# Performance work log

Hardware: AMD Instinct MI355X
Metric: run time of the kernel (lower is better)

The kernel has to match this reference:

```python
import jax, jax.numpy as jnp
import numpy as np

DIM = 384
NUM_HEADS = 12
WS = 7
POSMLP_DIM = 32
HEAD_DIM = DIM // NUM_HEADS
SCALE = HEAD_DIM ** -0.5


def setup_inputs() -> dict:
    key = jax.random.key(0)
    ks = jax.random.split(key, 10)
    B_ = 2048
    N = WS * WS
    nW = 64
    inp = {
        "x": jax.random.normal(ks[0], (B_, N, DIM), dtype=jnp.float32),
        "mask": jax.random.normal(ks[1], (nW, N, N), dtype=jnp.float32),
        # qkv Linear: weight [3*dim, dim], bias [3*dim]
        "qkv_w": jax.random.normal(ks[2], (3 * DIM, DIM), dtype=jnp.float32) * (DIM ** -0.5),
        "qkv_b": jax.random.normal(ks[3], (3 * DIM,), dtype=jnp.float32) * 0.02,
        # proj Linear
        "proj_w": jax.random.normal(ks[4], (DIM, DIM), dtype=jnp.float32) * (DIM ** -0.5),
        "proj_b": jax.random.normal(ks[5], (DIM,), dtype=jnp.float32) * 0.02,
        # posmlp: Conv2d(2, posmlp_dim, 1) -> ReLU -> Conv2d(posmlp_dim, num_heads, 1)
        "pm_w1": jax.random.normal(ks[6], (POSMLP_DIM, 2), dtype=jnp.float32) * 0.5,
        "pm_b1": jax.random.normal(ks[7], (POSMLP_DIM,), dtype=jnp.float32) * 0.02,
        "pm_w2": jax.random.normal(ks[8], (NUM_HEADS, POSMLP_DIM), dtype=jnp.float32) * (POSMLP_DIM ** -0.5),
        "pm_b2": jax.random.normal(ks[9], (NUM_HEADS,), dtype=jnp.float32) * 0.02,
    }
    return inp


def _pos_bias(pm_w1, pm_b1, pm_w2, pm_b2):
    # pos_hw: [2, N] with channel 0 = row index, channel 1 = col index
    coords = jnp.arange(WS, dtype=jnp.float32)
    pos_h = jnp.repeat(coords[:, None], WS, axis=1).reshape(-1)  # row idx
    pos_w = jnp.tile(coords[None, :], (WS, 1)).reshape(-1)       # col idx
    pos = jnp.stack([pos_h, pos_w], axis=0)                      # [2, N]
    # pos_input[c, i, j] = pos[c, j] - pos[c, i]  (unsqueeze(2) - unsqueeze(3))
    d = pos[:, None, :] - pos[:, :, None]                        # [2, N, N]
    d = jnp.sign(d) * jnp.log1p(jnp.abs(d))
    # 1x1 convs == per-position channel MLP
    h = jax.nn.relu(jnp.einsum("cij,oc->oij", d, pm_w1) + pm_b1[:, None, None])
    bias = jnp.einsum("cij,oc->oij", h, pm_w2) + pm_b2[:, None, None]  # [H, N, N]
    return bias


def reference(x, mask, qkv_w, qkv_b, proj_w, proj_b, pm_w1, pm_b1, pm_w2, pm_b2):
    B_, N, C = x.shape
    H = NUM_HEADS
    qkv = x @ qkv_w.T + qkv_b                                     # [B_, N, 3C]
    qkv = qkv.reshape(B_, N, 3, H, C // H).transpose(2, 0, 3, 1, 4)
    q, k, v = qkv[0], qkv[1], qkv[2]                              # [B_, H, N, d]
    attn = jnp.einsum("bhnd,bhmd->bhnm", q * SCALE, k)            # [B_, H, N, N]
    attn = attn + _pos_bias(pm_w1, pm_b1, pm_w2, pm_b2)[None]
    nW = mask.shape[0]
    attn = attn.reshape(B_ // nW, nW, H, N, N) + mask[None, :, None]
    attn = jax.nn.softmax(attn.reshape(B_, H, N, N), axis=-1)
    out = jnp.einsum("bhnm,bhmd->bhnd", attn, v)                  # [B_, H, N, d]
    out = out.transpose(0, 2, 1, 3).reshape(B_, N, C)
    return out @ proj_w.T + proj_b
```

## Files before the change

### kernel.cpp

```cpp
#include <hip/hip_runtime.h>
#include <hip/hip_bf16.h>
#include <stdint.h>

#define DIM 384
#define QKVN 1152
#define NHEAD 12
#define HDIM 32
#define NTOK 49
#define NWIN 2048
static constexpr float SCALE_Q = 0.17677669529663687f;

typedef float f32x4 __attribute__((ext_vector_type(4)));
typedef float f32x4u __attribute__((ext_vector_type(4), aligned(4)));
typedef __bf16 bf16x8 __attribute__((ext_vector_type(8)));
typedef unsigned short u16;
typedef u16 u16x8 __attribute__((ext_vector_type(8)));
typedef u16 u16x4 __attribute__((ext_vector_type(4)));

static __device__ __forceinline__ u16 f2bf(float f) {
  __hip_bfloat16 h = __float2bfloat16(f);
  return __builtin_bit_cast(unsigned short, h);
}
static __device__ __forceinline__ f32x4 mfma_bf16(u16x8 a, u16x8 b, f32x4 c) {
  return __builtin_amdgcn_mfma_f32_16x16x32_bf16(
      __builtin_bit_cast(bf16x8, a), __builtin_bit_cast(bf16x8, b), c, 0, 0, 0);
}

__global__ void k_convert(const float* __restrict__ s, u16* __restrict__ d, int n) {
  int i = (blockIdx.x * 256 + threadIdx.x) * 4;
  if (i < n) {
    f32x4 v = *(const f32x4*)(s + i);
    u16x4 o;
    o[0] = f2bf(v[0]); o[1] = f2bf(v[1]); o[2] = f2bf(v[2]); o[3] = f2bf(v[3]);
    *(u16x4*)(d + i) = o;
  }
}

__global__ void k_posbias(const float* __restrict__ w1, const float* __restrict__ b1,
                          const float* __restrict__ w2, const float* __restrict__ b2,
                          float* __restrict__ out) {
  int idx = blockIdx.x * 256 + threadIdx.x;
  if (idx >= NTOK * NTOK) return;
  int i = idx / NTOK, j = idx % NTOK;
  float d0 = (float)(j / 7 - i / 7);
  float d1 = (float)(j % 7 - i % 7);
  d0 = copysignf(log1pf(fabsf(d0)), d0);
  d1 = copysignf(log1pf(fabsf(d1)), d1);
  float acc[NHEAD];
#pragma unroll
  for (int o2 = 0; o2 < NHEAD; o2++) acc[o2] = b2[o2];
#pragma unroll 4
  for (int o = 0; o < 32; o++) {
    float h = fmaxf(d0 * w1[o * 2] + d1 * w1[o * 2 + 1] + b1[o], 0.f);
#pragma unroll
    for (int o2 = 0; o2 < NHEAD; o2++) acc[o2] += h * w2[o2 * 32 + o];
  }
#pragma unroll
  for (int o2 = 0; o2 < NHEAD; o2++) out[(o2 * NTOK + i) * NTOK + j] = acc[o2];
}

__global__ void k_pbm(const float* __restrict__ posb, const float* __restrict__ mask,
                      float* __restrict__ pbm) {
  int idx = blockIdx.x * 256 + threadIdx.x;
  if (idx >= 64 * NHEAD * NTOK * NTOK) return;
  int j = idx % (NTOK * NTOK);
  int t = idx / (NTOK * NTOK);
  int h = t % NHEAD, w = t / NHEAD;
  pbm[idx] = posb[h * NTOK * NTOK + j] + mask[w * NTOK * NTOK + j];
}

template <int MODE>
__global__ __launch_bounds__(256) void k_gemm(const void* __restrict__ Ap,
                                              const u16* __restrict__ Bw,
                                              const float* __restrict__ bias,
                                              void* __restrict__ Cp) {
  __shared__ u16 As[128 * 32];
  __shared__ u16 Bs[128 * 32];
  const int tid = threadIdx.x;
  const int NB = (MODE == 0) ? 9 : 3;
  const int PER = (MODE == 0) ? 882 : 294;
  const int g = blockIdx.x;
  const int flat = (g & 7) * PER + (g >> 3);
  const int bm = flat / NB, bn = flat % NB;

  const int lane = tid & 63, wv = tid >> 6;
  const int wr = wv >> 1, wc = wv & 1;
  const int l15 = lane & 15, l4 = lane >> 4;
  const int srow = tid >> 1, sp = tid & 1;
  const int fS = (srow >> 1) & 3;
  const int ws0 = (2 * sp) ^ fS, ws1 = (2 * sp + 1) ^ fS;
  const int fr = (l15 >> 1) & 3;
  f32x4 acc[4][4] = {};

  f32x4 fA0, fA1, fA2, fA3;
  u16x8 rA0, rA1, rB0, rB1;

#define GLOAD(K0)                                                                   \
  {                                                                                 \
    if (MODE == 0) {                                                                \
      const float* ap = (const float*)Ap + (size_t)(bm * 128 + srow) * DIM + (K0) + sp * 16; \
      fA0 = *(const f32x4*)(ap);                                                    \
      fA1 = *(const f32x4*)(ap + 4);                                                \
      fA2 = *(const f32x4*)(ap + 8);                                                \
      fA3 = *(const f32x4*)(ap + 12);                                               \
    } else {                                                                        \
      const u16* ap = (const u16*)Ap + (size_t)(bm * 128 + srow) * DIM + (K0) + sp * 16; \
      rA0 = *(const u16x8*)ap;                                                      \
      rA1 = *(const u16x8*)(ap + 8);                                                \
    }                                                                               \
    const u16* bp = Bw + (size_t)(bn * 128 + srow) * DIM + (K0) + sp * 16;          \
    rB0 = *(const u16x8*)bp;                                                        \
    rB1 = *(const u16x8*)(bp + 8);                                                  \
  }

  GLOAD(0)
  const int NK = DIM / 32;
  for (int it = 0; it < NK; ++it) {
    u16x8 wa0, wa1, wb0, wb1;
    if (MODE == 0) {
#pragma unroll
      for (int j = 0; j < 4; j++) {
        wa0[j] = f2bf(fA0[j]); wa0[j + 4] = f2bf(fA1[j]);
        wa1[j] = f2bf(fA2[j]); wa1[j + 4] = f2bf(fA3[j]);
      }
    } else {
      wa0 = rA0; wa1 = rA1;
    }
    wb0 = rB0; wb1 = rB1;

    __syncthreads();
    *(u16x8*)&As[srow * 32 + ws0 * 8] = wa0;
    *(u16x8*)&As[srow * 32 + ws1 * 8] = wa1;
    *(u16x8*)&Bs[srow * 32 + ws0 * 8] = wb0;
    *(u16x8*)&Bs[srow * 32 + ws1 * 8] = wb1;
    __syncthreads();

    if (it + 1 < NK) GLOAD((it + 1) * 32)

    u16x8 af[4], bfr[4];
#pragma unroll
    for (int m = 0; m < 4; m++)
      af[m] = *(const u16x8*)&As[(wr * 64 + m * 16 + l15) * 32 + (l4 ^ fr) * 8];
#pragma unroll
    for (int n = 0; n < 4; n++)
      bfr[n] = *(const u16x8*)&Bs[(wc * 64 + n * 16 + l15) * 32 + (l4 ^ fr) * 8];
#pragma unroll
    for (int m = 0; m < 4; m++)
#pragma unroll
      for (int n = 0; n < 4; n++)
        acc[m][n] = mfma_bf16(af[m], bfr[n], acc[m][n]);
  }
#undef GLOAD

#pragma unroll
  for (int n = 0; n < 4; n++) {
    const int col = bn * 128 + wc * 64 + n * 16 + l15;
    const float bv = bias[col];
#pragma unroll
    for (int m = 0; m < 4; m++) {
      const int row0 = bm * 128 + wr * 64 + m * 16 + l4 * 4;
#pragma unroll
      for (int r = 0; r < 4; r++) {
        float v = acc[m][n][r] + bv;
        if (MODE == 0) {
          if (col < DIM) v *= SCALE_Q;
          ((u16*)Cp)[(size_t)(row0 + r) * QKVN + col] = f2bf(v);
        } else {
          ((float*)Cp)[(size_t)(row0 + r) * DIM + col] = v;
        }
      }
    }
  }
}

__global__ __launch_bounds__(256) void k_attn(const u16* __restrict__ qkv,
                                              const float* __restrict__ pbm,
                                              u16* __restrict__ aout) {
  __shared__ u16 qs[2][64 * 32];
  __shared__ u16 ks[2][64 * 32];
  __shared__ u16 vts[2][32 * 72];
  __shared__ u16 ps[64 * 72];
  const int g = blockIdx.x;
  const int b = (((g >> 3) >> 3) << 6) + (g & 7) * 8 + ((g >> 3) & 7);
  const int w = b & 63;
  const int tid = threadIdx.x;
  const int lane = tid & 63, wv = tid >> 6;
  const int l15 = lane & 15, l4 = lane >> 4;
  const int fr = (l15 >> 1) & 3;

  for (int i = tid; i < 64 * 32; i += 256)
    if ((i >> 5) >= NTOK) { qs[0][i] = 0; qs[1][i] = 0; ks[0][i] = 0; ks[1][i] = 0; }
  for (int i = tid; i < 32 * 72; i += 256)
    if ((i % 72) >= NTOK) { vts[0][i] = 0; vts[1][i] = 0; }

  const int trow = tid >> 2, tseg = tid & 3;
  const int fT = (trow >> 1) & 3;
  u16x8 rq, rk, rv;

#define LOAD_REGS(h)                                                                 \
  if (tid < 196) {                                                                   \
    const u16* src = qkv + (size_t)(b * NTOK + trow) * QKVN + (h) * HDIM + tseg * 8; \
    rq = *(const u16x8*)src;                                                         \
    rk = *(const u16x8*)(src + DIM);                                                 \
    rv = *(const u16x8*)(src + 2 * DIM);                                             \
  }
#define WRITE_LDS(buf)                                                               \
  if (tid < 196) {                                                                   \
    *(u16x8*)&qs[buf][trow * 32 + (tseg ^ fT) * 8] = rq;                             \
    *(u16x8*)&ks[buf][trow * 32 + (tseg ^ fT) * 8] = rk;                             \
    _Pragma("unroll") for (int j = 0; j < 8; j++)                                    \
        vts[buf][(tseg * 8 + j) * 72 + trow] = rv[j];                                \
  }

  LOAD_REGS(0)
  WRITE_LDS(0)

  const int qrow = wv * 16 + l15;
  const int qc = (qrow < NTOK) ? qrow : NTOK - 1;

  for (int h = 0; h < NHEAD; ++h) {
    const int buf = h & 1;
    if (h + 1 < NHEAD) LOAD_REGS(h + 1)
    __syncthreads();

    u16x8 bq = *(const u16x8*)&qs[buf][(wv * 16 + l15) * 32 + (l4 ^ fr) * 8];
    f32x4 s[4];
#pragma unroll
    for (int n = 0; n < 4; n++) {
      u16x8 ak = *(const u16x8*)&ks[buf][(n * 16 + l15) * 32 + (l4 ^ fr) * 8];
      f32x4 z = {0.f, 0.f, 0.f, 0.f};
      s[n] = mfma_bf16(ak, bq, z);
    }

    const float* pr = pbm + ((size_t)(w * NHEAD + h) * NTOK + qc) * NTOK;
    float sv[4][4];
    float mx = -1e30f;
#pragma unroll
    for (int n = 0; n < 4; n++) {
      f32x4 p4 = *(const f32x4u*)(pr + n * 16 + l4 * 4);
#pragma unroll
      for (int r = 0; r < 4; r++) {
        const int k = n * 16 + l4 * 4 + r;
        float v = (k < NTOK) ? s[n][r] + p4[r] : -1e30f;
        sv[n][r] = v;
        mx = fmaxf(mx, v);
      }
    }
    mx = fmaxf(mx, __shfl_xor(mx, 16));
    mx = fmaxf(mx, __shfl_xor(mx, 32));
    float e[4][4], sum = 0.f;
#pragma unroll
    for (int n = 0; n < 4; n++)
#pragma unroll
      for (int r = 0; r < 4; r++) {
        const int k = n * 16 + l4 * 4 + r;
        e[n][r] = (k < NTOK) ? __expf(sv[n][r] - mx) : 0.f;
        sum += e[n][r];
      }
    sum += __shfl_xor(sum, 16);
    sum += __shfl_xor(sum, 32);
    const float inv = 1.0f / sum;
#pragma unroll
    for (int n = 0; n < 4; n++) {
      u16x4 pk;
#pragma unroll
      for (int r = 0; r < 4; r++) pk[r] = f2bf(e[n][r] * inv);
      *(u16x4*)&ps[qrow * 72 + n * 16 + l4 * 4] = pk;
    }

    f32x4 o[2] = {};
#pragma unroll
    for (int kk = 0; kk < 2; kk++) {
      u16x8 ap = *(const u16x8*)&ps[(wv * 16 + l15) * 72 + kk * 32 + l4 * 8];
#pragma unroll
      for (int n = 0; n < 2; n++) {
        u16x8 bvv = *(const u16x8*)&vts[buf][(n * 16 + l15) * 72 + kk * 32 + l4 * 8];
        o[n] = mfma_bf16(ap, bvv, o[n]);
      }
    }
#pragma unroll
    for (int n = 0; n < 2; n++) {
      const int col = n * 16 + l15;
#pragma unroll
      for (int r = 0; r < 4; r++) {
        const int row = wv * 16 + l4 * 4 + r;
        if (row < NTOK)
          aout[(size_t)(b * NTOK + row) * DIM + h * HDIM + col] = f2bf(o[n][r]);
      }
    }
    if (h + 1 < NHEAD) WRITE_LDS(buf ^ 1)
  }
#undef LOAD_REGS
#undef WRITE_LDS
}

extern "C" void kernel_launch(void* const* d_in, const int* in_sizes, int n_in,
                              void* d_out, int out_size, void* d_ws, size_t ws_size,
                              hipStream_t stream) {
  const float* x      = (const float*)d_in[0];
  const float* mask   = (const float*)d_in[1];
  const float* qkv_w  = (const float*)d_in[2];
  const float* qkv_b  = (const float*)d_in[3];
  const float* proj_w = (const float*)d_in[4];
  const float* proj_b = (const float*)d_in[5];
  const float* pm_w1  = (const float*)d_in[6];
  const float* pm_b1  = (const float*)d_in[7];
  const float* pm_w2  = (const float*)d_in[8];
  const float* pm_b2  = (const float*)d_in[9];
  float* out = (float*)d_out;

  char* ws = (char*)d_ws;
  u16*   qkv   = (u16*)(ws + 0);
  u16*   wqkv  = (u16*)(ws + 231211008);
  u16*   wproj = (u16*)(ws + 232095744);
  float* posb  = (float*)(ws + 232390656);
  float* pbm   = (float*)(ws + 232505904);
  u16*   aout  = (u16*)(ws + 239881776);

  k_convert<<<432, 256, 0, stream>>>(qkv_w, wqkv, 442368);
  k_convert<<<144, 256, 0, stream>>>(proj_w, wproj, 147456);
  k_posbias<<<10, 256, 0, stream>>>(pm_w1, pm_b1, pm_w2, pm_b2, posb);
  k_pbm<<<7203, 256, 0, stream>>>(posb, mask, pbm);
  k_gemm<0><<<7056, 256, 0, stream>>>((const void*)x, wqkv, qkv_b, (void*)qkv);
  k_attn<<<2048, 256, 0, stream>>>(qkv, pbm, aout);
  k_gemm<1><<<2352, 256, 0, stream>>>((const void*)aout, wproj, proj_b, (void*)out);
}
```

Baseline: 655.2 us.

## Restructure GEMM to hold full-K A tile in LDS and stream B from registers

The GEMM kernel now loads a 64-row slab of A across the entire K=384 into shared memory once, converting fp32 to bf16 only once per element. It then loops over all N column blocks inside the block, reading B fragments straight from global memory into registers with a one-step prefetch instead of staging them through LDS. This removes repeated A reloads and conversions across column blocks and drops per-K-step barriers, and launch bounds now request 3 blocks per CU. The cost is 48KB of LDS per block, fewer blocks in the grid, and B reads served from cache by every block without LDS sharing between waves.

```diff
diff --git a/kernel.cpp b/kernel.cpp
--- a/kernel.cpp
+++ b/kernel.cpp
@@ -70,103 +70,93 @@
 }
 
 template <int MODE>
-__global__ __launch_bounds__(256) void k_gemm(const void* __restrict__ Ap,
-                                              const u16* __restrict__ Bw,
-                                              const float* __restrict__ bias,
-                                              void* __restrict__ Cp) {
-  __shared__ u16 As[128 * 32];
-  __shared__ u16 Bs[128 * 32];
+__global__ __launch_bounds__(256, 3) void k_gemm(const void* __restrict__ Ap,
+                                                 const u16* __restrict__ Bw,
+                                                 const float* __restrict__ bias,
+                                                 void* __restrict__ Cp) {
+  __shared__ u16 As[64 * 384];
   const int tid = threadIdx.x;
-  const int NB = (MODE == 0) ? 9 : 3;
-  const int PER = (MODE == 0) ? 882 : 294;
-  const int g = blockIdx.x;
-  const int flat = (g & 7) * PER + (g >> 3);
-  const int bm = flat / NB, bn = flat % NB;
-
+  const int bm = blockIdx.x;
   const int lane = tid & 63, wv = tid >> 6;
-  const int wr = wv >> 1, wc = wv & 1;
   const int l15 = lane & 15, l4 = lane >> 4;
-  const int srow = tid >> 1, sp = tid & 1;
-  const int fS = (srow >> 1) & 3;
-  const int ws0 = (2 * sp) ^ fS, ws1 = (2 * sp + 1) ^ fS;
-  const int fr = (l15 >> 1) & 3;
-  f32x4 acc[4][4] = {};
-
-  f32x4 fA0, fA1, fA2, fA3;
-  u16x8 rA0, rA1, rB0, rB1;
-
-#define GLOAD(K0)                                                                   \
-  {                                                                                 \
-    if (MODE == 0) {                                                                \
-      const float* ap = (const float*)Ap + (size_t)(bm * 128 + srow) * DIM + (K0) + sp * 16; \
-      fA0 = *(const f32x4*)(ap);                                                    \
-      fA1 = *(const f32x4*)(ap + 4);                                                \
-      fA2 = *(const f32x4*)(ap + 8);                                                \
-      fA3 = *(const f32x4*)(ap + 12);                                               \
-    } else {                                                                        \
-      const u16* ap = (const u16*)Ap + (size_t)(bm * 128 + srow) * DIM + (K0) + sp * 16; \
-      rA0 = *(const u16x8*)ap;                                                      \
-      rA1 = *(const u16x8*)(ap + 8);                                                \
-    }                                                                               \
-    const u16* bp = Bw + (size_t)(bn * 128 + srow) * DIM + (K0) + sp * 16;          \
-    rB0 = *(const u16x8*)bp;                                                        \
-    rB1 = *(const u16x8*)(bp + 8);                                                  \
-  }
-
-  GLOAD(0)
-  const int NK = DIM / 32;
-  for (int it = 0; it < NK; ++it) {
-    u16x8 wa0, wa1, wb0, wb1;
+
+  {
+    const int sr = tid >> 2;
+    const int s0 = (tid & 3) * 12;
     if (MODE == 0) {
-#pragma unroll
-      for (int j = 0; j < 4; j++) {
-        wa0[j] = f2bf(fA0[j]); wa0[j + 4] = f2bf(fA1[j]);
-        wa1[j] = f2bf(fA2[j]); wa1[j + 4] = f2bf(fA3[j]);
+      const float* ap = (const float*)Ap + (size_t)(bm * 64 + sr) * DIM + s0 * 8;
+      f32x4 f[24];
+#pragma unroll
+      for (int i = 0; i < 24; i++) f[i] = *(const f32x4*)(ap + i * 4);
+#pragma unroll
+      for (int s = 0; s < 12; s++) {
+        u16x8 o;
+#pragma unroll
+        for (int j = 0; j < 4; j++) { o[j] = f2bf(f[2 * s][j]); o[j + 4] = f2bf(f[2 * s + 1][j]); }
+        const int seg = s0 + s, g = seg >> 2, l = seg & 3;
+        *(u16x8*)&As[sr * 384 + g * 32 + ((l ^ (sr & 3)) * 8)] = o;
       }
     } else {
-      wa0 = rA0; wa1 = rA1;
-    }
-    wb0 = rB0; wb1 = rB1;
-
-    __syncthreads();
-    *(u16x8*)&As[srow * 32 + ws0 * 8] = wa0;
-    *(u16x8*)&As[srow * 32 + ws1 * 8] = wa1;
-    *(u16x8*)&Bs[srow * 32 + ws0 * 8] = wb0;
-    *(u16x8*)&Bs[srow * 32 + ws1 * 8] = wb1;
-    __syncthreads();
-
-    if (it + 1 < NK) GLOAD((it + 1) * 32)
-
-    u16x8 af[4], bfr[4];
-#pragma unroll
-    for (int m = 0; m < 4; m++)
-      af[m] = *(const u16x8*)&As[(wr * 64 + m * 16 + l15) * 32 + (l4 ^ fr) * 8];
-#pragma unroll
-    for (int n = 0; n < 4; n++)
-      bfr[n] = *(const u16x8*)&Bs[(wc * 64 + n * 16 + l15) * 32 + (l4 ^ fr) * 8];
-#pragma unroll
-    for (int m = 0; m < 4; m++)
-#pragma unroll
-      for (int n = 0; n < 4; n++)
-        acc[m][n] = mfma_bf16(af[m], bfr[n], acc[m][n]);
-  }
-#undef GLOAD
-
-#pragma unroll
-  for (int n = 0; n < 4; n++) {
-    const int col = bn * 128 + wc * 64 + n * 16 + l15;
-    const float bv = bias[col];
-#pragma unroll
-    for (int m = 0; m < 4; m++) {
-      const int row0 = bm * 128 + wr * 64 + m * 16 + l4 * 4;
-#pragma unroll
-      for (int r = 0; r < 4; r++) {
-        float v = acc[m][n][r] + bv;
-        if (MODE == 0) {
-          if (col < DIM) v *= SCALE_Q;
-          ((u16*)Cp)[(size_t)(row0 + r) * QKVN + col] = f2bf(v);
-        } else {
-          ((float*)Cp)[(size_t)(row0 + r) * DIM + col] = v;
+      const u16* ap = (const u16*)Ap + (size_t)(bm * 64 + sr) * DIM + s0 * 8;
+#pragma unroll
+      for (int s = 0; s < 12; s++) {
+        u16x8 v = *(const u16x8*)(ap + s * 8);
+        const int seg = s0 + s, g = seg >> 2, l = seg & 3;
+        *(u16x8*)&As[sr * 384 + g * 32 + ((l ^ (sr & 3)) * 8)] = v;
+      }
+    }
+  }
+  __syncthreads();
+
+  const int NBN = (MODE == 0) ? 9 : 3;
+
+  const u16* bbase = Bw + (size_t)(wv * 32 + l15) * DIM + l4 * 8;
+
+  u16x8 nb0 = *(const u16x8*)(bbase);
+  u16x8 nb1 = *(const u16x8*)(bbase + 16 * DIM);
+
+  for (int bn = 0; bn < NBN; ++bn) {
+    f32x4 acc[4][2] = {};
+    const u16* bcur = bbase + (size_t)bn * 128 * DIM;
+#pragma unroll
+    for (int it = 0; it < 12; ++it) {
+      u16x8 b0 = nb0, b1 = nb1;
+      if (it < 11) {
+        nb0 = *(const u16x8*)(bcur + (it + 1) * 32);
+        nb1 = *(const u16x8*)(bcur + 16 * DIM + (it + 1) * 32);
+      } else if (bn + 1 < NBN) {
+        const u16* bnx = bbase + (size_t)(bn + 1) * 128 * DIM;
+        nb0 = *(const u16x8*)(bnx);
+        nb1 = *(const u16x8*)(bnx + 16 * DIM);
+      }
+      u16x8 af[4];
+#pragma unroll
+      for (int m = 0; m < 4; m++) {
+        const int r = m * 16 + l15;
+        af[m] = *(const u16x8*)&As[r * 384 + it * 32 + ((l4 ^ (r & 3)) * 8)];
+      }
+#pragma unroll
+      for (int m = 0; m < 4; m++) {
+        acc[m][0] = mfma_bf16(af[m], b0, acc[m][0]);
+        acc[m][1] = mfma_bf16(af[m], b1, acc[m][1]);
+      }
+    }
+#pragma unroll
+    for (int n = 0; n < 2; n++) {
+      const int col = bn * 128 + wv * 32 + n * 16 + l15;
+      const float bv = bias[col];
+#pragma unroll
+      for (int m = 0; m < 4; m++) {
+        const int row0 = bm * 64 + m * 16 + l4 * 4;
+#pragma unroll
+        for (int r = 0; r < 4; r++) {
+          float v = acc[m][n][r] + bv;
+          if (MODE == 0) {
+            if (col < DIM) v *= SCALE_Q;
+            ((u16*)Cp)[(size_t)(row0 + r) * QKVN + col] = f2bf(v);
+          } else {
+            ((float*)Cp)[(size_t)(row0 + r) * DIM + col] = v;
+          }
         }
       }
     }
@@ -321,7 +311,7 @@
   k_convert<<<144, 256, 0, stream>>>(proj_w, wproj, 147456);
   k_posbias<<<10, 256, 0, stream>>>(pm_w1, pm_b1, pm_w2, pm_b2, posb);
   k_pbm<<<7203, 256, 0, stream>>>(posb, mask, pbm);
-  k_gemm<0><<<7056, 256, 0, stream>>>((const void*)x, wqkv, qkv_b, (void*)qkv);
+  k_gemm<0><<<1568, 256, 0, stream>>>((const void*)x, wqkv, qkv_b, (void*)qkv);
   k_attn<<<2048, 256, 0, stream>>>(qkv, pbm, aout);
-  k_gemm<1><<<2352, 256, 0, stream>>>((const void*)aout, wproj, proj_b, (void*)out);
-}
+  k_gemm<1><<<1568, 256, 0, stream>>>((const void*)aout, wproj, proj_b, (void*)out);
+}
```

Result: slower. 991.4 us (+51.3%).

## Double-buffer GEMM LDS with BK=64 and stage bias rows in attention LDS

Applied to the files above, without the earlier changes.

The GEMM kernels now use a K tile of 64 with double-buffered LDS, so global loads for the next tile overlap the MFMAs on the current one and only one barrier is needed per iteration. They also use an XOR swizzle over 8 segments and are wrapped in separate kernels with launch_bounds(256,2). The attention kernel cooperatively loads each head's 49x49 pos-bias+mask block into padded LDS, double-buffered alongside q/k/v, replacing per-lane unaligned global reads. The cost is more LDS (64KB per GEMM block) and more registers, which can limit occupancy.

```diff
diff --git a/kernel.cpp b/kernel.cpp
--- a/kernel.cpp
+++ b/kernel.cpp
@@ -70,12 +70,12 @@
 }
 
 template <int MODE>
-__global__ __launch_bounds__(256) void k_gemm(const void* __restrict__ Ap,
-                                              const u16* __restrict__ Bw,
-                                              const float* __restrict__ bias,
-                                              void* __restrict__ Cp) {
-  __shared__ u16 As[128 * 32];
-  __shared__ u16 Bs[128 * 32];
+static __device__ __forceinline__ void gemm_body(const void* __restrict__ Ap,
+                                                 const u16* __restrict__ Bw,
+                                                 const float* __restrict__ bias,
+                                                 void* __restrict__ Cp) {
+  __shared__ u16 As[2][128 * 64];
+  __shared__ u16 Bs[2][128 * 64];
   const int tid = threadIdx.x;
   const int NB = (MODE == 0) ? 9 : 3;
   const int PER = (MODE == 0) ? 882 : 294;
@@ -86,71 +86,75 @@
   const int lane = tid & 63, wv = tid >> 6;
   const int wr = wv >> 1, wc = wv & 1;
   const int l15 = lane & 15, l4 = lane >> 4;
-  const int srow = tid >> 1, sp = tid & 1;
-  const int fS = (srow >> 1) & 3;
-  const int ws0 = (2 * sp) ^ fS, ws1 = (2 * sp + 1) ^ fS;
-  const int fr = (l15 >> 1) & 3;
+  const int sr = tid >> 1, hp = tid & 1;
+
+  const float* a0 = (const float*)Ap + (size_t)(bm * 128 + sr) * DIM + hp * 32;
+  const u16*   a1 = (const u16*)Ap + (size_t)(bm * 128 + sr) * DIM + hp * 32;
+  const u16*   bb = Bw + (size_t)(bn * 128 + sr) * DIM + hp * 32;
+
+  f32x4 fA[8];
+  u16x8 rA[4], rB[4];
+
+#define GLOAD(K0)                                                        \
+  {                                                                      \
+    if (MODE == 0) {                                                     \
+      _Pragma("unroll") for (int i = 0; i < 8; i++)                      \
+          fA[i] = *(const f32x4*)(a0 + (K0) + i * 4);                    \
+    } else {                                                             \
+      _Pragma("unroll") for (int i = 0; i < 4; i++)                      \
+          rA[i] = *(const u16x8*)(a1 + (K0) + i * 8);                    \
+    }                                                                    \
+    _Pragma("unroll") for (int i = 0; i < 4; i++)                        \
+        rB[i] = *(const u16x8*)(bb + (K0) + i * 8);                      \
+  }
+
+#define WLDS(BUF)                                                        \
+  {                                                                      \
+    _Pragma("unroll") for (int s = 0; s < 4; s++) {                      \
+      u16x8 av;                                                          \
+      if (MODE == 0) {                                                   \
+        _Pragma("unroll") for (int j = 0; j < 4; j++) {                  \
+          av[j] = f2bf(fA[2 * s][j]);                                    \
+          av[j + 4] = f2bf(fA[2 * s + 1][j]);                            \
+        }                                                                \
+      } else av = rA[s];                                                 \
+      const int st = ((hp * 4 + s) ^ (sr & 7)) * 8;                      \
+      *(u16x8*)&As[BUF][sr * 64 + st] = av;                              \
+      *(u16x8*)&Bs[BUF][sr * 64 + st] = rB[s];                           \
+    }                                                                    \
+  }
+
+  GLOAD(0)
+  WLDS(0)
   f32x4 acc[4][4] = {};
 
-  f32x4 fA0, fA1, fA2, fA3;
-  u16x8 rA0, rA1, rB0, rB1;
-
-#define GLOAD(K0)                                                                   \
-  {                                                                                 \
-    if (MODE == 0) {                                                                \
-      const float* ap = (const float*)Ap + (size_t)(bm * 128 + srow) * DIM + (K0) + sp * 16; \
-      fA0 = *(const f32x4*)(ap);                                                    \
-      fA1 = *(const f32x4*)(ap + 4);                                                \
-      fA2 = *(const f32x4*)(ap + 8);                                                \
-      fA3 = *(const f32x4*)(ap + 12);                                               \
-    } else {                                                                        \
-      const u16* ap = (const u16*)Ap + (size_t)(bm * 128 + srow) * DIM + (K0) + sp * 16; \
-      rA0 = *(const u16x8*)ap;                                                      \
-      rA1 = *(const u16x8*)(ap + 8);                                                \
-    }                                                                               \
-    const u16* bp = Bw + (size_t)(bn * 128 + srow) * DIM + (K0) + sp * 16;          \
-    rB0 = *(const u16x8*)bp;                                                        \
-    rB1 = *(const u16x8*)(bp + 8);                                                  \
-  }
-
-  GLOAD(0)
-  const int NK = DIM / 32;
-  for (int it = 0; it < NK; ++it) {
-    u16x8 wa0, wa1, wb0, wb1;
-    if (MODE == 0) {
-#pragma unroll
-      for (int j = 0; j < 4; j++) {
-        wa0[j] = f2bf(fA0[j]); wa0[j + 4] = f2bf(fA1[j]);
-        wa1[j] = f2bf(fA2[j]); wa1[j + 4] = f2bf(fA3[j]);
-      }
-    } else {
-      wa0 = rA0; wa1 = rA1;
-    }
-    wb0 = rB0; wb1 = rB1;
-
+  for (int it = 0; it < 6; ++it) {
+    const int cur = it & 1;
+    if (it < 5) GLOAD((it + 1) * 64)
     __syncthreads();
-    *(u16x8*)&As[srow * 32 + ws0 * 8] = wa0;
-    *(u16x8*)&As[srow * 32 + ws1 * 8] = wa1;
-    *(u16x8*)&Bs[srow * 32 + ws0 * 8] = wb0;
-    *(u16x8*)&Bs[srow * 32 + ws1 * 8] = wb1;
-    __syncthreads();
-
-    if (it + 1 < NK) GLOAD((it + 1) * 32)
-
-    u16x8 af[4], bfr[4];
-#pragma unroll
-    for (int m = 0; m < 4; m++)
-      af[m] = *(const u16x8*)&As[(wr * 64 + m * 16 + l15) * 32 + (l4 ^ fr) * 8];
-#pragma unroll
-    for (int n = 0; n < 4; n++)
-      bfr[n] = *(const u16x8*)&Bs[(wc * 64 + n * 16 + l15) * 32 + (l4 ^ fr) * 8];
-#pragma unroll
-    for (int m = 0; m < 4; m++)
-#pragma unroll
-      for (int n = 0; n < 4; n++)
-        acc[m][n] = mfma_bf16(af[m], bfr[n], acc[m][n]);
+#pragma unroll
+    for (int kk = 0; kk < 2; ++kk) {
+      u16x8 af[4], bfr[4];
+#pragma unroll
+      for (int m = 0; m < 4; m++) {
+        const int row = wr * 64 + m * 16 + l15;
+        af[m] = *(const u16x8*)&As[cur][row * 64 + (((kk * 4 + l4) ^ (l15 & 7)) * 8)];
+      }
+#pragma unroll
+      for (int n = 0; n < 4; n++) {
+        const int row = wc * 64 + n * 16 + l15;
+        bfr[n] = *(const u16x8*)&Bs[cur][row * 64 + (((kk * 4 + l4) ^ (l15 & 7)) * 8)];
+      }
+#pragma unroll
+      for (int m = 0; m < 4; m++)
+#pragma unroll
+        for (int n = 0; n < 4; n++)
+          acc[m][n] = mfma_bf16(af[m], bfr[n], acc[m][n]);
+    }
+    if (it < 5) WLDS(cur ^ 1)
   }
 #undef GLOAD
+#undef WLDS
 
 #pragma unroll
   for (int n = 0; n < 4; n++) {
@@ -173,12 +177,26 @@
   }
 }
 
+__global__ __launch_bounds__(256, 2) void k_qkv(const float* __restrict__ Ap,
+                                                const u16* __restrict__ Bw,
+                                                const float* __restrict__ bias,
+                                                u16* __restrict__ Cp) {
+  gemm_body<0>(Ap, Bw, bias, Cp);
+}
+__global__ __launch_bounds__(256, 2) void k_proj(const u16* __restrict__ Ap,
+                                                 const u16* __restrict__ Bw,
+                                                 const float* __restrict__ bias,
+                                                 float* __restrict__ Cp) {
+  gemm_body<1>(Ap, Bw, bias, Cp);
+}
+
 __global__ __launch_bounds__(256) void k_attn(const u16* __restrict__ qkv,
                                               const float* __restrict__ pbm,
                                               u16* __restrict__ aout) {
   __shared__ u16 qs[2][64 * 32];
   __shared__ u16 ks[2][64 * 32];
   __shared__ u16 vts[2][32 * 72];
+  __shared__ float pbs[2][49 * 52 + 16];
   __shared__ u16 ps[64 * 72];
   const int g = blockIdx.x;
   const int b = (((g >> 3) >> 3) << 6) + (g & 7) * 8 + ((g >> 3) & 7);
@@ -197,19 +215,41 @@
   const int fT = (trow >> 1) & 3;
   u16x8 rq, rk, rv;
 
+  int psrc[3], pdst[3];
+  bool pvld[3];
+#pragma unroll
+  for (int j = 0; j < 3; j++) {
+    const int i = tid + j * 256;
+    pvld[j] = i < 637;
+    const int r = pvld[j] ? (i / 13) : 0;
+    const int c = pvld[j] ? (i - r * 13) : 0;
+    psrc[j] = r * 49 + c * 4;
+    pdst[j] = r * 52 + c * 4;
+  }
+  f32x4u pb[3];
+
 #define LOAD_REGS(h)                                                                 \
-  if (tid < 196) {                                                                   \
-    const u16* src = qkv + (size_t)(b * NTOK + trow) * QKVN + (h) * HDIM + tseg * 8; \
-    rq = *(const u16x8*)src;                                                         \
-    rk = *(const u16x8*)(src + DIM);                                                 \
-    rv = *(const u16x8*)(src + 2 * DIM);                                             \
+  {                                                                                  \
+    if (tid < 196) {                                                                 \
+      const u16* src = qkv + (size_t)(b * NTOK + trow) * QKVN + (h) * HDIM + tseg * 8; \
+      rq = *(const u16x8*)src;                                                       \
+      rk = *(const u16x8*)(src + DIM);                                               \
+      rv = *(const u16x8*)(src + 2 * DIM);                                           \
+    }                                                                                \
+    const float* pbase = pbm + (size_t)(w * NHEAD + (h)) * (NTOK * NTOK);            \
+    _Pragma("unroll") for (int j = 0; j < 3; j++)                                    \
+        if (pvld[j]) pb[j] = *(const f32x4u*)(pbase + psrc[j]);                      \
   }
 #define WRITE_LDS(buf)                                                               \
-  if (tid < 196) {                                                                   \
-    *(u16x8*)&qs[buf][trow * 32 + (tseg ^ fT) * 8] = rq;                             \
-    *(u16x8*)&ks[buf][trow * 32 + (tseg ^ fT) * 8] = rk;                             \
-    _Pragma("unroll") for (int j = 0; j < 8; j++)                                    \
-        vts[buf][(tseg * 8 + j) * 72 + trow] = rv[j];                                \
+  {                                                                                  \
+    if (tid < 196) {                                                                 \
+      *(u16x8*)&qs[buf][trow * 32 + (tseg ^ fT) * 8] = rq;                           \
+      *(u16x8*)&ks[buf][trow * 32 + (tseg ^ fT) * 8] = rk;                           \
+      _Pragma("unroll") for (int j = 0; j < 8; j++)                                  \
+          vts[buf][(tseg * 8 + j) * 72 + trow] = rv[j];                              \
+    }                                                                                \
+    _Pragma("unroll") for (int j = 0; j < 3; j++)                                    \
+        if (pvld[j]) *(f32x4*)&pbs[buf][pdst[j]] = pb[j];                            \
   }
 
   LOAD_REGS(0)
@@ -232,12 +272,12 @@
       s[n] = mfma_bf16(ak, bq, z);
     }
 
-    const float* pr = pbm + ((size_t)(w * NHEAD + h) * NTOK + qc) * NTOK;
+    const float* pl = &pbs[buf][qc * 52];
     float sv[4][4];
     float mx = -1e30f;
 #pragma unroll
     for (int n = 0; n < 4; n++) {
-      f32x4 p4 = *(const f32x4u*)(pr + n * 16 + l4 * 4);
+      f32x4 p4 = *(const f32x4*)(pl + n * 16 + l4 * 4);
 #pragma unroll
       for (int r = 0; r < 4; r++) {
         const int k = n * 16 + l4 * 4 + r;
@@ -321,7 +361,7 @@
   k_convert<<<144, 256, 0, stream>>>(proj_w, wproj, 147456);
   k_posbias<<<10, 256, 0, stream>>>(pm_w1, pm_b1, pm_w2, pm_b2, posb);
   k_pbm<<<7203, 256, 0, stream>>>(posb, mask, pbm);
-  k_gemm<0><<<7056, 256, 0, stream>>>((const void*)x, wqkv, qkv_b, (void*)qkv);
+  k_qkv<<<7056, 256, 0, stream>>>(x, wqkv, qkv_b, qkv);
   k_attn<<<2048, 256, 0, stream>>>(qkv, pbm, aout);
-  k_gemm<1><<<2352, 256, 0, stream>>>((const void*)aout, wproj, proj_b, (void*)out);
-}
+  k_proj<<<2352, 256, 0, stream>>>(aout, wproj, proj_b, out);
+}
```

Result: slower. 670.0 us (+2.3%).
